# Kernel tuning notes

Measured on AMD Instinct MI355X. Metric: run time of the kernel, lower is better.

The kernel has to match this reference:

```python
import jax, jax.numpy as jnp
import numpy as np

N_HEAD = 12
SCALING = 0.17677669529663687  # 1/sqrt(head_dim=32)


def setup_inputs() -> dict:
    key = jax.random.key(0)
    ks = jax.random.split(key, 6)
    B, R, C, E = 1, 256, 384, 384
    s = 1.0 / np.sqrt(E)
    return {
        "x": jax.random.normal(ks[0], (B, R, C, E), dtype=jnp.float32),
        "Wq": (jax.random.normal(ks[1], (E, E), dtype=jnp.float32) * s),
        "Wk": (jax.random.normal(ks[2], (E, E), dtype=jnp.float32) * s),
        "Wv": (jax.random.normal(ks[3], (E, E), dtype=jnp.float32) * s),
        "Wq_s": (jax.random.normal(ks[4], (E, E), dtype=jnp.float32) * s),
        "Wk_s": (jax.random.normal(ks[5], (E, E), dtype=jnp.float32) * s),
        "res_mask": jnp.ones((B, C), dtype=jnp.int32),
        "seq_mask": jnp.ones((B, R), dtype=jnp.int32),
    }


def reference(x, Wq, Wk, Wv, Wq_s, Wk_s, res_mask, seq_mask):
    B, R, C, E = x.shape
    H = N_HEAD
    D = E // H
    NEG = jnp.finfo(x.dtype).min

    # ---- SeqWeightAttention: per-column attention over rows, query = row 0 ----
    scale_s = 1.0 / np.sqrt(D)
    msa = jnp.transpose(x, (0, 2, 1, 3))                 # [B,C,R,E]
    q0 = msa[:, :, 0]                                    # [B,C,E]
    Qs = (q0 @ Wq_s).reshape(B, C, 1, H, D)
    Qs = jnp.transpose(Qs, (0, 1, 3, 2, 4)) * scale_s    # [B,C,H,1,D]
    Ks = (msa @ Wk_s).reshape(B, C, R, H, D)
    Ks = jnp.transpose(Ks, (0, 1, 3, 4, 2))              # [B,C,H,D,R]
    QKs = Qs @ Ks                                        # [B,C,H,1,R]
    QKs = jnp.where(seq_mask[:, None, None, None, :] == 0, NEG, QKs)
    sw = jax.nn.softmax(QKs, axis=-1)
    sw = jnp.transpose(sw, (0, 4, 1, 2, 3))              # [B,R,C,H,1]

    # ---- main attention, row-contracted (attn_seq_weight path) ----
    scaling = SCALING / np.sqrt(C)                        # seqlen_scaling=True
    Q = (x @ Wq).reshape(B, R, C, H, D) * scaling * sw    # Q modulated by seq weights
    K = (x @ Wk).reshape(B, R, C, H, D)
    V = (x @ Wv).reshape(B, R, C, H, D)

    QK = jnp.einsum('brihd,brjhd->bhij', Q, K)            # contract rows + head_dim
    rm = res_mask[:, :, None] * res_mask[:, None, :]      # [B,C,C]
    QK = jnp.where(rm[:, None, :, :] == 0, NEG, QK)
    attn = jax.nn.softmax(QK, axis=-1)                    # [B,H,C,C]

    out = jnp.einsum('bhij,brjhd->brihd', attn, V)
    return out.reshape(B, R, C, E)
```

## Files before the change

kernel.cpp:

```cpp
#include <hip/hip_runtime.h>
#include <math.h>
#include <stdint.h>

#define DEV_INLINE __device__ __forceinline__

constexpr int R_ = 256, C_ = 384, E_ = 384, H_ = 12, D_ = 32;
constexpr float NEGF = -3.402823466e38f;

typedef __attribute__((ext_vector_type(4))) float f32x4;
typedef __attribute__((ext_vector_type(8))) short short8;
typedef __attribute__((ext_vector_type(4))) unsigned short u16x4;

constexpr size_t o_qs     = 0;
constexpr size_t o_p      = o_qs + (size_t)C_ * E_;
constexpr size_t o_logits = o_p + (size_t)C_ * H_ * E_;
constexpr size_t o_sw     = o_logits + (size_t)C_ * H_ * R_;
constexpr size_t o_attn   = o_sw + (size_t)C_ * H_ * R_;
constexpr size_t o_q3     = o_attn + (size_t)H_ * C_ * C_;
constexpr size_t SZBIG  = 75497472;
constexpr size_t ob_q3b = o_q3 * 4;
constexpr size_t ob_k3b = ob_q3b + SZBIG;
constexpr size_t ob_v3b = ob_k3b + SZBIG;
constexpr size_t ob_xb  = ob_v3b + SZBIG;
constexpr size_t QKSZ   = 7077888;

DEV_INLINE unsigned short bf16h(float x) {
  unsigned int u = __builtin_bit_cast(unsigned int, x);
  unsigned int r = (u + 0x7FFFu + ((u >> 16) & 1u)) >> 16;
  return (unsigned short)r;
}
DEV_INLINE float waveRedMax(float v) {
#pragma unroll
  for (int o = 32; o > 0; o >>= 1) v = fmaxf(v, __shfl_down(v, o));
  return v;
}
DEV_INLINE float waveRedSum(float v) {
#pragma unroll
  for (int o = 32; o > 0; o >>= 1) v += __shfl_down(v, o);
  return v;
}

DEV_INLINE void gll16(const void* g, void* l) {
  __builtin_amdgcn_global_load_lds(
      reinterpret_cast<__attribute__((address_space(1))) void*>(
          reinterpret_cast<uintptr_t>(g)),
      reinterpret_cast<__attribute__((address_space(3))) void*>(
          reinterpret_cast<uintptr_t>(l)),
      16, 0, 0);
}

template <int ROWS, int UPR, int MASK, int SHIFT>
DEV_INLINE void stageT(const unsigned short* __restrict__ g, int lda,
                       unsigned short* l) {
  int t = threadIdx.x, w = t >> 6, lane = t & 63;
  constexpr int NI = (ROWS * UPR) / 64;
  constexpr int PW = NI / 4;
#pragma unroll
  for (int j = 0; j < PW; ++j) {
    int u0 = (w * PW + j) * 64;
    int u = u0 + lane;
    int row = u / UPR, qp = u % UPR;
    int q = qp ^ ((row >> SHIFT) & MASK);
    gll16(g + (size_t)row * lda + q * 8, l + (size_t)u0 * 8);
  }
}

template <int MASK, int SHIFT>
DEV_INLINE short8 fragLd(const unsigned short* base, int row, int q, int rowShorts) {
  int qp = q ^ ((row >> SHIFT) & MASK);
  return *(const short8*)(base + row * rowShorts + qp * 8);
}

__global__ void k_prep(const float* __restrict__ x, const float* __restrict__ Wq,
                       const float* __restrict__ Wk, const float* __restrict__ Wv,
                       unsigned short* __restrict__ xb, unsigned short* __restrict__ Wtb) {
  int bid = blockIdx.x, t = threadIdx.x;
  if (bid < 6144) {
    size_t i = ((size_t)bid * 384 + t) * 16;
    unsigned short h[16];
#pragma unroll
    for (int j = 0; j < 4; ++j) {
      float4 f = *(const float4*)&x[i + j * 4];
      h[j * 4 + 0] = bf16h(f.x);
      h[j * 4 + 1] = bf16h(f.y);
      h[j * 4 + 2] = bf16h(f.z);
      h[j * 4 + 3] = bf16h(f.w);
    }
    *(short8*)&xb[i] = *(const short8*)&h[0];
    *(short8*)&xb[i + 8] = *(const short8*)&h[8];
  } else {
    int n = bid - 6144;
    const float* W;
    int col;
    if (n < 384)      { W = Wq; col = n; }
    else if (n < 768) { W = Wk; col = n - 384; }
    else              { W = Wv; col = n - 768; }
    Wtb[(size_t)n * 384 + t] = bf16h(W[(size_t)t * 384 + col]);
  }
}

__global__ __launch_bounds__(256) void k_logits_sm(
    const float* __restrict__ x, const unsigned short* __restrict__ xb,
    const float* __restrict__ Wq_s, const float* __restrict__ Wk_s,
    const int* __restrict__ seq_mask, float* __restrict__ swT) {
  int c = blockIdx.x, t = threadIdx.x;
  __shared__ float xq[384], qs_l[384];
  __shared__ unsigned short pB[16 * 392];
  __shared__ unsigned short sA[256 * 32];
  __shared__ float lg[12 * 256];
  __shared__ float red[4];
  int w = t >> 6, lane = t & 63, id16 = lane & 15, g = lane >> 4;

  for (int k = t; k < 384; k += 256) xq[k] = x[(size_t)c * 384 + k];
  __syncthreads();
  for (int e = t; e < 384; e += 256) {
    float s = 0.f;
    for (int k = 0; k < 384; ++k) s += xq[k] * Wq_s[(size_t)k * 384 + e];
    qs_l[e] = s * 0.17677669529663687f;
  }
  __syncthreads();
  for (int idx = t; idx < 4608; idx += 256) {
    int h = idx / 384, kk = idx - h * 384;
    const float* wrow = &Wk_s[(size_t)kk * 384 + h * 32];
    const float* qv = &qs_l[h * 32];
    float s = 0.f;
#pragma unroll
    for (int d = 0; d < 32; d += 4) {
      float4 wv = *(const float4*)&wrow[d];
      s += wv.x * qv[d] + wv.y * qv[d + 1] + wv.z * qv[d + 2] + wv.w * qv[d + 3];
    }
    pB[h * 392 + kk] = bf16h(s);
  }
  for (int i = t + 12 * 392; i < 16 * 392; i += 256) pB[i] = 0;
  __syncthreads();

  f32x4 acc[4];
#pragma unroll
  for (int mi = 0; mi < 4; ++mi) acc[mi] = (f32x4){0.f, 0.f, 0.f, 0.f};
  for (int k0 = 0; k0 < 384; k0 += 32) {
    stageT<256, 4, 3, 0>(xb + (size_t)c * 384 + k0, 384 * 384, sA);
    __syncthreads();
    short8 Bf = *(const short8*)(pB + id16 * 392 + k0 + g * 8);
#pragma unroll
    for (int mi = 0; mi < 4; ++mi) {
      short8 Af = fragLd<3, 0>(sA, w * 64 + mi * 16 + id16, g, 32);
      acc[mi] = __builtin_amdgcn_mfma_f32_16x16x32_bf16(Af, Bf, acc[mi], 0, 0, 0);
    }
    __syncthreads();
  }
  int l4 = (lane >> 4) * 4;
#pragma unroll
  for (int mi = 0; mi < 4; ++mi) {
    if (id16 < 12) {
      f32x4 a = acc[mi];
#pragma unroll
      for (int reg = 0; reg < 4; ++reg)
        lg[id16 * 256 + w * 64 + mi * 16 + l4 + reg] = a[reg];
    }
  }
  __syncthreads();
  int wid = t >> 6;
  const float scal = 0.17677669529663687f / sqrtf((float)C_);
  bool masked = (seq_mask[t] == 0);
  for (int h = 0; h < 12; ++h) {
    float v = masked ? NEGF : lg[h * 256 + t];
    float m = waveRedMax(v);
    if ((t & 63) == 0) red[wid] = m;
    __syncthreads();
    float mx = fmaxf(fmaxf(red[0], red[1]), fmaxf(red[2], red[3]));
    __syncthreads();
    float e = expf(v - mx);
    float s = waveRedSum(e);
    if ((t & 63) == 0) red[wid] = s;
    __syncthreads();
    float sum = red[0] + red[1] + red[2] + red[3];
    swT[((size_t)h * 256 + t) * 384 + c] = e / sum * scal;
    __syncthreads();
  }
}

__global__ __launch_bounds__(256, 4) void k_proj_all(
    const unsigned short* __restrict__ xb, const unsigned short* __restrict__ Wtb,
    const float* __restrict__ swT, unsigned short* __restrict__ Q3b,
    unsigned short* __restrict__ K3b, unsigned short* __restrict__ V3b) {
  __shared__ __align__(16) unsigned short smem[2 * 128 * 64];
  unsigned short* sA = smem;
  unsigned short* sB = smem + 128 * 64;
  int Dd = blockIdx.x;
  int L = (Dd & 7) * 864 + (Dd >> 3);
  int bm = L / 9, bn = L - bm * 9;
  int n0 = bn * 128, m0 = bm * 128;
  int wave = threadIdx.x >> 6, wr = wave >> 1, wc = wave & 1;
  int lane = threadIdx.x & 63, id16 = lane & 15, g = lane >> 4;
  f32x4 acc[4][4];
#pragma unroll
  for (int mi = 0; mi < 4; ++mi)
#pragma unroll
    for (int ni = 0; ni < 4; ++ni) acc[mi][ni] = (f32x4){0.f, 0.f, 0.f, 0.f};

  for (int it = 0; it < 6; ++it) {
    stageT<128, 8, 7, 0>(xb + (size_t)m0 * 384 + it * 64, 384, sA);
    stageT<128, 8, 7, 0>(Wtb + (size_t)n0 * 384 + it * 64, 384, sB);
    __syncthreads();
    short8 Af[4][2], Bf[4][2];
#pragma unroll
    for (int mi = 0; mi < 4; ++mi) {
      int row = wr * 64 + mi * 16 + id16;
#pragma unroll
      for (int kk = 0; kk < 2; ++kk) Af[mi][kk] = fragLd<7, 0>(sA, row, kk * 4 + g, 64);
    }
#pragma unroll
    for (int ni = 0; ni < 4; ++ni) {
      int col = wc * 64 + ni * 16 + id16;
#pragma unroll
      for (int kk = 0; kk < 2; ++kk) Bf[ni][kk] = fragLd<7, 0>(sB, col, kk * 4 + g, 64);
    }
#pragma unroll
    for (int kk = 0; kk < 2; ++kk)
#pragma unroll
      for (int mi = 0; mi < 4; ++mi)
#pragma unroll
        for (int ni = 0; ni < 4; ++ni)
          acc[mi][ni] = __builtin_amdgcn_mfma_f32_16x16x32_bf16(Af[mi][kk], Bf[ni][kk],
                                                                acc[mi][ni], 0, 0, 0);
    __syncthreads();
  }

  int l4 = (lane >> 4) * 4;
  int r = bm / 3, cb = (bm % 3) * 128;
  if (bn < 6) {
    bool isQ = bn < 3;
    int hbase = isQ ? bn * 4 : (bn - 3) * 4;
#pragma unroll
    for (int mi = 0; mi < 4; ++mi) {
      int clBase = wr * 64 + mi * 16 + l4;
#pragma unroll
      for (int ni = 0; ni < 4; ++ni) {
        int nl = wc * 64 + ni * 16 + id16;
        int hhl = nl >> 5, d = nl & 31;
        f32x4 a = acc[mi][ni];
        if (isQ) {
          float4 sv =
              *(const float4*)&swT[((size_t)(hbase + hhl) * 256 + r) * 384 + cb + clBase];
          a[0] *= sv.x; a[1] *= sv.y; a[2] *= sv.z; a[3] *= sv.w;
        }
#pragma unroll
        for (int reg = 0; reg < 4; ++reg)
          smem[hhl * 4096 + (clBase + reg) * 32 + d] = bf16h(a[reg]);
      }
    }
    __syncthreads();
    unsigned short* dst = isQ ? Q3b : K3b;
#pragma unroll
    for (int seg = 0; seg < 8; ++seg) {
      int off = seg * 2048 + threadIdx.x * 8;
      int hhl = off >> 12, inner = off & 4095;
      int hg = hbase + hhl;
      *(short8*)(dst + (((size_t)hg * 256 + r) * 384 + cb) * 32 + inner) =
          *(const short8*)(smem + off);
    }
  } else {
    int hbase = (bn - 6) * 4;
#pragma unroll
    for (int mi = 0; mi < 4; ++mi) {
      int clBase = wr * 64 + mi * 16 + l4;
#pragma unroll
      for (int ni = 0; ni < 4; ++ni) {
        int nl = wc * 64 + ni * 16 + id16;
        int hhl = nl >> 5, d = nl & 31;
        int cg = clBase ^ ((d & 7) << 2);
        f32x4 a = acc[mi][ni];
        u16x4 hv;
#pragma unroll
        for (int reg = 0; reg < 4; ++reg) hv[reg] = bf16h(a[reg]);
        *(u16x4*)(smem + hhl * 4096 + d * 128 + cg) = hv;
      }
    }
    __syncthreads();
#pragma unroll
    for (int seg = 0; seg < 16; ++seg) {
      int Lg = seg * 1024 + threadIdx.x * 4;
      int hhl = Lg >> 12, rem = Lg & 4095, d = rem >> 7, cc = rem & 127;
      int cp = cc ^ ((d & 7) << 2);
      u16x4 v = *(const u16x4*)(smem + hhl * 4096 + d * 128 + cp);
      int hg = hbase + hhl;
      *(u16x4*)(V3b + ((size_t)hg * 8192 + r * 32 + d) * 384 + cb + cc) = v;
    }
  }
}

__global__ __launch_bounds__(256, 4) void k_qk_mma(
    const unsigned short* __restrict__ Q3b, const unsigned short* __restrict__ K3b,
    float* __restrict__ QKf0, float* __restrict__ QKf1,
    float* __restrict__ QKf2, float* __restrict__ QKf3) {
  __shared__ unsigned short sA[2 * 4096], sB[2 * 4096];
  int Dd = blockIdx.x;
  int L = (Dd & 7) * 54 + (Dd >> 3);
  int kh = L / 108, rem = L - kh * 108;
  int h = rem / 9, r2 = rem - h * 9, bi = r2 / 3, bj = r2 - bi * 3;
  int i0 = bi * 128, j0 = bj * 128;
  int wave = threadIdx.x >> 6, wr = wave >> 1, wc = wave & 1;
  int lane = threadIdx.x & 63, id16 = lane & 15, g = lane >> 4;
  f32x4 acc[4][4];
#pragma unroll
  for (int mi = 0; mi < 4; ++mi)
#pragma unroll
    for (int ni = 0; ni < 4; ++ni) acc[mi][ni] = (f32x4){0.f, 0.f, 0.f, 0.f};

  for (int it = 0; it < 32; ++it) {
    int r = kh * 64 + it * 2;
#pragma unroll
    for (int rr = 0; rr < 2; ++rr) {
      stageT<128, 4, 3, 1>(Q3b + (((size_t)h * 256 + r + rr) * 384 + i0) * 32, 32,
                           sA + rr * 4096);
      stageT<128, 4, 3, 1>(K3b + (((size_t)h * 256 + r + rr) * 384 + j0) * 32, 32,
                           sB + rr * 4096);
    }
    __syncthreads();
#pragma unroll
    for (int rr = 0; rr < 2; ++rr) {
      short8 Af[4], Bf[4];
#pragma unroll
      for (int mi = 0; mi < 4; ++mi)
        Af[mi] = fragLd<3, 1>(sA + rr * 4096, wr * 64 + mi * 16 + id16, g, 32);
#pragma unroll
      for (int ni = 0; ni < 4; ++ni)
        Bf[ni] = fragLd<3, 1>(sB + rr * 4096, wc * 64 + ni * 16 + id16, g, 32);
#pragma unroll
      for (int mi = 0; mi < 4; ++mi)
#pragma unroll
        for (int ni = 0; ni < 4; ++ni)
          acc[mi][ni] = __builtin_amdgcn_mfma_f32_16x16x32_bf16(Af[mi], Bf[ni],
                                                                acc[mi][ni], 0, 0, 0);
    }
    __syncthreads();
  }
  int l4 = (lane >> 4) * 4;
  float* dst = (kh == 0) ? QKf0 : (kh == 1) ? QKf1 : (kh == 2) ? QKf2 : QKf3;
#pragma unroll
  for (int mi = 0; mi < 4; ++mi)
#pragma unroll
    for (int ni = 0; ni < 4; ++ni) {
      int ii = i0 + wr * 64 + mi * 16 + l4;
      int j = j0 + wc * 64 + ni * 16 + id16;
      f32x4 a = acc[mi][ni];
#pragma unroll
      for (int reg = 0; reg < 4; ++reg)
        dst[((size_t)h * 384 + ii + reg) * 384 + j] = a[reg];
    }
}

__global__ void k_softmax_j(const int* __restrict__ res_mask, const float* __restrict__ QKf0,
                            const float* __restrict__ QKf1, const float* __restrict__ QKf2,
                            const float* __restrict__ QKf3,
                            unsigned short* __restrict__ attnb) {
  int i = blockIdx.x, h = blockIdx.y, t = threadIdx.x;
  int lane = t & 63, wid = t >> 6;
  size_t base = ((size_t)h * C_ + i) * C_;
  float v = (QKf0[base + t] + QKf1[base + t]) + (QKf2[base + t] + QKf3[base + t]);
  if ((res_mask[i] * res_mask[t]) == 0) v = NEGF;
  __shared__ float red[6];
  float m = waveRedMax(v);
  if (lane == 0) red[wid] = m;
  __syncthreads();
  float mx = red[0];
#pragma unroll
  for (int w = 1; w < 6; ++w) mx = fmaxf(mx, red[w]);
  __syncthreads();
  float e = expf(v - mx);
  float s = waveRedSum(e);
  if (lane == 0) red[wid] = s;
  __syncthreads();
  float sum = 0.f;
#pragma unroll
  for (int w = 0; w < 6; ++w) sum += red[w];
  attnb[base + t] = bf16h(e / sum);
}

__global__ __launch_bounds__(256, 4) void k_out_mma(
    const unsigned short* __restrict__ attnb, const unsigned short* __restrict__ V3b,
    float* __restrict__ out) {
  __shared__ __align__(16) unsigned short smem[2 * 128 * 64];
  unsigned short* sA = smem;
  unsigned short* sB = smem + 128 * 64;
  int Dd = blockIdx.x;
  int L = (Dd & 7) * 288 + (Dd >> 3);
  int bn = L % 64, bm = (L / 64) % 3, h = L / 192;
  int n0 = bn * 128, m0 = bm * 128;
  int wave = threadIdx.x >> 6, wr = wave >> 1, wc = wave & 1;
  int lane = threadIdx.x & 63, id16 = lane & 15, g = lane >> 4;
  f32x4 acc[4][4];
#pragma unroll
  for (int mi = 0; mi < 4; ++mi)
#pragma unroll
    for (int ni = 0; ni < 4; ++ni) acc[mi][ni] = (f32x4){0.f, 0.f, 0.f, 0.f};
  const unsigned short* Ab = attnb + (size_t)h * 384 * 384 + (size_t)m0 * 384;
  const unsigned short* Bb = V3b + (size_t)h * 8192 * 384 + (size_t)n0 * 384;

  for (int it = 0; it < 6; ++it) {
    stageT<128, 8, 7, 0>(Ab + it * 64, 384, sA);
    stageT<128, 8, 7, 0>(Bb + it * 64, 384, sB);
    __syncthreads();
    short8 Af[4][2], Bf[4][2];
#pragma unroll
    for (int mi = 0; mi < 4; ++mi) {
      int row = wr * 64 + mi * 16 + id16;
#pragma unroll
      for (int kk = 0; kk < 2; ++kk) Af[mi][kk] = fragLd<7, 0>(sA, row, kk * 4 + g, 64);
    }
#pragma unroll
    for (int ni = 0; ni < 4; ++ni) {
      int col = wc * 64 + ni * 16 + id16;
#pragma unroll
      for (int kk = 0; kk < 2; ++kk) Bf[ni][kk] = fragLd<7, 0>(sB, col, kk * 4 + g, 64);
    }
#pragma unroll
    for (int kk = 0; kk < 2; ++kk)
#pragma unroll
      for (int mi = 0; mi < 4; ++mi)
#pragma unroll
        for (int ni = 0; ni < 4; ++ni)
          acc[mi][ni] = __builtin_amdgcn_mfma_f32_16x16x32_bf16(Af[mi][kk], Bf[ni][kk],
                                                                acc[mi][ni], 0, 0, 0);
    __syncthreads();
  }

  int l4 = (lane >> 4) * 4;
  float* smf = (float*)smem;
#pragma unroll
  for (int p = 0; p < 2; ++p) {
#pragma unroll
    for (int mi = 0; mi < 4; ++mi) {
      int iL = wr * 64 + mi * 16 + l4;
#pragma unroll
      for (int nq = 0; nq < 2; ++nq) {
        int ni = 2 * p + nq;
        int d = nq * 16 + id16;
        f32x4 a = acc[mi][ni];
#pragma unroll
        for (int reg = 0; reg < 4; ++reg)
          smf[wc * 4096 + (iL + reg) * 32 + d] = a[reg];
      }
    }
    __syncthreads();
#pragma unroll
    for (int seg = 0; seg < 8; ++seg) {
      int o = seg * 1024 + threadIdx.x * 4;
      int plane = o >> 12, rest = o & 4095;
      int iL = rest >> 5, d = rest & 31;
      int rg = (n0 >> 5) + plane * 2 + p;
      *(float4*)&out[(((size_t)rg * 384 + m0 + iL) * 12 + h) * 32 + d] =
          *(const float4*)&smf[o];
    }
    __syncthreads();
  }
}

extern "C" void kernel_launch(void* const* d_in, const int* in_sizes, int n_in,
                              void* d_out, int out_size, void* d_ws, size_t ws_size,
                              hipStream_t stream) {
  const float* x = (const float*)d_in[0];
  const float* Wq = (const float*)d_in[1];
  const float* Wk = (const float*)d_in[2];
  const float* Wv = (const float*)d_in[3];
  const float* Wq_s = (const float*)d_in[4];
  const float* Wk_s = (const float*)d_in[5];
  const int* res_mask = (const int*)d_in[6];
  const int* seq_mask = (const int*)d_in[7];
  float* ws = (float*)d_ws;
  char* wsb = (char*)d_ws;
  float* out = (float*)d_out;

  float* swT          = ws + o_logits;
  unsigned short* Wtb = (unsigned short*)(wsb + o_attn * 4);
  float* QKf0         = ws + o_attn;
  unsigned short* Q3b = (unsigned short*)(wsb + ob_q3b);
  unsigned short* K3b = (unsigned short*)(wsb + ob_k3b);
  unsigned short* V3b = (unsigned short*)(wsb + ob_v3b);
  unsigned short* xb  = (unsigned short*)(wsb + ob_xb);
  unsigned short* attnb = Q3b;
  float* QKf1 = (float*)(wsb + ob_xb);
  float* QKf2 = (float*)(wsb + ob_xb + QKSZ);
  float* QKf3 = (float*)(wsb + ob_xb + 2 * QKSZ);

  hipLaunchKernelGGL(k_prep, dim3(7296), dim3(384), 0, stream, x, Wq, Wk, Wv, xb, Wtb);
  hipLaunchKernelGGL(k_logits_sm, dim3(C_), dim3(256), 0, stream, x, xb, Wq_s, Wk_s,
                     seq_mask, swT);
  hipLaunchKernelGGL(k_proj_all, dim3(6912), dim3(256), 0, stream, xb, Wtb, swT,
                     Q3b, K3b, V3b);
  hipLaunchKernelGGL(k_qk_mma, dim3(432), dim3(256), 0, stream, Q3b, K3b,
                     QKf0, QKf1, QKf2, QKf3);
  hipLaunchKernelGGL(k_softmax_j, dim3(C_, H_), dim3(C_), 0, stream, res_mask,
                     QKf0, QKf1, QKf2, QKf3, attnb);
  hipLaunchKernelGGL(k_out_mma, dim3(2304), dim3(256), 0, stream, attnb, V3b, out);
}
```

Measured before the change: 358.5 us.

## Store QK partials as bf16 and retile out GEMM to full-row attention tiles

The QK split-K partial sums are now written as bf16 rather than fp32, which halves the traffic between the QK kernel and the softmax kernel. The cost is extra rounding error on the logits before they are summed. The output GEMM is also retiled: each block now keeps all 384 attention rows in LDS against a 64-column slice of V, with 32-wide K steps and a 6x4 accumulator per wave. This stops re-reading V tiles across row blocks, but it uses more registers and lowers launch bounds occupancy to 3.

```diff
diff --git a/kernel.cpp b/kernel.cpp
--- a/kernel.cpp
+++ b/kernel.cpp
@@ -11,9 +11,7 @@
 typedef __attribute__((ext_vector_type(8))) short short8;
 typedef __attribute__((ext_vector_type(4))) unsigned short u16x4;
 
-constexpr size_t o_qs     = 0;
-constexpr size_t o_p      = o_qs + (size_t)C_ * E_;
-constexpr size_t o_logits = o_p + (size_t)C_ * H_ * E_;
+constexpr size_t o_logits = (size_t)C_ * E_ + (size_t)C_ * H_ * E_;
 constexpr size_t o_sw     = o_logits + (size_t)C_ * H_ * R_;
 constexpr size_t o_attn   = o_sw + (size_t)C_ * H_ * R_;
 constexpr size_t o_q3     = o_attn + (size_t)H_ * C_ * C_;
@@ -22,12 +20,15 @@
 constexpr size_t ob_k3b = ob_q3b + SZBIG;
 constexpr size_t ob_v3b = ob_k3b + SZBIG;
 constexpr size_t ob_xb  = ob_v3b + SZBIG;
-constexpr size_t QKSZ   = 7077888;
+constexpr size_t PSZ    = 3538944;
 
 DEV_INLINE unsigned short bf16h(float x) {
   unsigned int u = __builtin_bit_cast(unsigned int, x);
   unsigned int r = (u + 0x7FFFu + ((u >> 16) & 1u)) >> 16;
   return (unsigned short)r;
+}
+DEV_INLINE float b2f(unsigned short u) {
+  return __builtin_bit_cast(float, ((unsigned int)u) << 16);
 }
 DEV_INLINE float waveRedMax(float v) {
 #pragma unroll
@@ -291,8 +292,8 @@
 
 __global__ __launch_bounds__(256, 4) void k_qk_mma(
     const unsigned short* __restrict__ Q3b, const unsigned short* __restrict__ K3b,
-    float* __restrict__ QKf0, float* __restrict__ QKf1,
-    float* __restrict__ QKf2, float* __restrict__ QKf3) {
+    unsigned short* __restrict__ P0, unsigned short* __restrict__ P1,
+    unsigned short* __restrict__ P2, unsigned short* __restrict__ P3) {
   __shared__ unsigned short sA[2 * 4096], sB[2 * 4096];
   int Dd = blockIdx.x;
   int L = (Dd & 7) * 54 + (Dd >> 3);
@@ -336,7 +337,7 @@
     __syncthreads();
   }
   int l4 = (lane >> 4) * 4;
-  float* dst = (kh == 0) ? QKf0 : (kh == 1) ? QKf1 : (kh == 2) ? QKf2 : QKf3;
+  unsigned short* dst = (kh == 0) ? P0 : (kh == 1) ? P1 : (kh == 2) ? P2 : P3;
 #pragma unroll
   for (int mi = 0; mi < 4; ++mi)
 #pragma unroll
@@ -346,18 +347,21 @@
       f32x4 a = acc[mi][ni];
 #pragma unroll
       for (int reg = 0; reg < 4; ++reg)
-        dst[((size_t)h * 384 + ii + reg) * 384 + j] = a[reg];
-    }
-}
-
-__global__ void k_softmax_j(const int* __restrict__ res_mask, const float* __restrict__ QKf0,
-                            const float* __restrict__ QKf1, const float* __restrict__ QKf2,
-                            const float* __restrict__ QKf3,
+        dst[((size_t)h * 384 + ii + reg) * 384 + j] = bf16h(a[reg]);
+    }
+}
+
+__global__ void k_softmax_j(const int* __restrict__ res_mask,
+                            const unsigned short* __restrict__ P0,
+                            const unsigned short* __restrict__ P1,
+                            const unsigned short* __restrict__ P2,
+                            const unsigned short* __restrict__ P3,
                             unsigned short* __restrict__ attnb) {
   int i = blockIdx.x, h = blockIdx.y, t = threadIdx.x;
   int lane = t & 63, wid = t >> 6;
   size_t base = ((size_t)h * C_ + i) * C_;
-  float v = (QKf0[base + t] + QKf1[base + t]) + (QKf2[base + t] + QKf3[base + t]);
+  float v = (b2f(P0[base + t]) + b2f(P1[base + t])) +
+            (b2f(P2[base + t]) + b2f(P3[base + t]));
   if ((res_mask[i] * res_mask[t]) == 0) v = NEGF;
   __shared__ float red[6];
   float m = waveRedMax(v);
@@ -377,79 +381,71 @@
   attnb[base + t] = bf16h(e / sum);
 }
 
-__global__ __launch_bounds__(256, 4) void k_out_mma(
+__global__ __launch_bounds__(256, 3) void k_out_mma(
     const unsigned short* __restrict__ attnb, const unsigned short* __restrict__ V3b,
     float* __restrict__ out) {
-  __shared__ __align__(16) unsigned short smem[2 * 128 * 64];
+  __shared__ __align__(16) unsigned short smem[16384];
   unsigned short* sA = smem;
-  unsigned short* sB = smem + 128 * 64;
+  unsigned short* sB = smem + 12288;
   int Dd = blockIdx.x;
-  int L = (Dd & 7) * 288 + (Dd >> 3);
-  int bn = L % 64, bm = (L / 64) % 3, h = L / 192;
-  int n0 = bn * 128, m0 = bm * 128;
-  int wave = threadIdx.x >> 6, wr = wave >> 1, wc = wave & 1;
+  int L = (Dd & 7) * 192 + (Dd >> 3);
+  int h = L >> 7, rdt = L & 127;
+  int w = threadIdx.x >> 6;
   int lane = threadIdx.x & 63, id16 = lane & 15, g = lane >> 4;
-  f32x4 acc[4][4];
-#pragma unroll
-  for (int mi = 0; mi < 4; ++mi)
-#pragma unroll
-    for (int ni = 0; ni < 4; ++ni) acc[mi][ni] = (f32x4){0.f, 0.f, 0.f, 0.f};
-  const unsigned short* Ab = attnb + (size_t)h * 384 * 384 + (size_t)m0 * 384;
-  const unsigned short* Bb = V3b + (size_t)h * 8192 * 384 + (size_t)n0 * 384;
-
-  for (int it = 0; it < 6; ++it) {
-    stageT<128, 8, 7, 0>(Ab + it * 64, 384, sA);
-    stageT<128, 8, 7, 0>(Bb + it * 64, 384, sB);
-    __syncthreads();
-    short8 Af[4][2], Bf[4][2];
-#pragma unroll
-    for (int mi = 0; mi < 4; ++mi) {
-      int row = wr * 64 + mi * 16 + id16;
-#pragma unroll
-      for (int kk = 0; kk < 2; ++kk) Af[mi][kk] = fragLd<7, 0>(sA, row, kk * 4 + g, 64);
-    }
-#pragma unroll
-    for (int ni = 0; ni < 4; ++ni) {
-      int col = wc * 64 + ni * 16 + id16;
-#pragma unroll
-      for (int kk = 0; kk < 2; ++kk) Bf[ni][kk] = fragLd<7, 0>(sB, col, kk * 4 + g, 64);
-    }
-#pragma unroll
-    for (int kk = 0; kk < 2; ++kk)
-#pragma unroll
-      for (int mi = 0; mi < 4; ++mi)
-#pragma unroll
-        for (int ni = 0; ni < 4; ++ni)
-          acc[mi][ni] = __builtin_amdgcn_mfma_f32_16x16x32_bf16(Af[mi][kk], Bf[ni][kk],
-                                                                acc[mi][ni], 0, 0, 0);
+  f32x4 acc[6][4];
+#pragma unroll
+  for (int mi = 0; mi < 6; ++mi)
+#pragma unroll
+    for (int nf = 0; nf < 4; ++nf) acc[mi][nf] = (f32x4){0.f, 0.f, 0.f, 0.f};
+  const unsigned short* Ab = attnb + (size_t)h * 147456;
+  const unsigned short* Bb = V3b + (size_t)h * 8192 * 384 + (size_t)(rdt * 64) * 384;
+
+  for (int it = 0; it < 12; ++it) {
+    stageT<384, 4, 3, 1>(Ab + it * 32, 384, sA);
+    stageT<64, 4, 3, 1>(Bb + it * 32, 384, sB);
+    __syncthreads();
+    short8 Af[6], Bf[4];
+#pragma unroll
+    for (int mi = 0; mi < 6; ++mi)
+      Af[mi] = fragLd<3, 1>(sA, w * 96 + mi * 16 + id16, g, 32);
+#pragma unroll
+    for (int nf = 0; nf < 4; ++nf)
+      Bf[nf] = fragLd<3, 1>(sB, nf * 16 + id16, g, 32);
+#pragma unroll
+    for (int mi = 0; mi < 6; ++mi)
+#pragma unroll
+      for (int nf = 0; nf < 4; ++nf)
+        acc[mi][nf] = __builtin_amdgcn_mfma_f32_16x16x32_bf16(Af[mi], Bf[nf],
+                                                              acc[mi][nf], 0, 0, 0);
     __syncthreads();
   }
 
   int l4 = (lane >> 4) * 4;
   float* smf = (float*)smem;
 #pragma unroll
-  for (int p = 0; p < 2; ++p) {
-#pragma unroll
-    for (int mi = 0; mi < 4; ++mi) {
-      int iL = wr * 64 + mi * 16 + l4;
-#pragma unroll
-      for (int nq = 0; nq < 2; ++nq) {
-        int ni = 2 * p + nq;
-        int d = nq * 16 + id16;
-        f32x4 a = acc[mi][ni];
+  for (int p = 0; p < 3; ++p) {
+#pragma unroll
+    for (int mi = 0; mi < 6; ++mi) {
+      int rb = w * 96 + mi * 16;
+      if ((rb >> 7) != p) continue;
+      int ibase = (rb & 127) + l4;
+#pragma unroll
+      for (int nf = 0; nf < 4; ++nf) {
+        int rdl = nf * 16 + id16;
+        f32x4 a = acc[mi][nf];
 #pragma unroll
         for (int reg = 0; reg < 4; ++reg)
-          smf[wc * 4096 + (iL + reg) * 32 + d] = a[reg];
+          smf[(ibase + reg) * 64 + rdl] = a[reg];
       }
     }
     __syncthreads();
 #pragma unroll
     for (int seg = 0; seg < 8; ++seg) {
       int o = seg * 1024 + threadIdx.x * 4;
-      int plane = o >> 12, rest = o & 4095;
-      int iL = rest >> 5, d = rest & 31;
-      int rg = (n0 >> 5) + plane * 2 + p;
-      *(float4*)&out[(((size_t)rg * 384 + m0 + iL) * 12 + h) * 32 + d] =
+      int il = o >> 6, rdl = o & 63;
+      int rg = rdt * 2 + (rdl >> 5), d = rdl & 31;
+      int i = p * 128 + il;
+      *(float4*)&out[(((size_t)rg * 384 + i) * 12 + h) * 32 + d] =
           *(const float4*)&smf[o];
     }
     __syncthreads();
@@ -473,24 +469,23 @@
 
   float* swT          = ws + o_logits;
   unsigned short* Wtb = (unsigned short*)(wsb + o_attn * 4);
-  float* QKf0         = ws + o_attn;
   unsigned short* Q3b = (unsigned short*)(wsb + ob_q3b);
   unsigned short* K3b = (unsigned short*)(wsb + ob_k3b);
   unsigned short* V3b = (unsigned short*)(wsb + ob_v3b);
   unsigned short* xb  = (unsigned short*)(wsb + ob_xb);
   unsigned short* attnb = Q3b;
-  float* QKf1 = (float*)(wsb + ob_xb);
-  float* QKf2 = (float*)(wsb + ob_xb + QKSZ);
-  float* QKf3 = (float*)(wsb + ob_xb + 2 * QKSZ);
+  unsigned short* P0 = (unsigned short*)(wsb + ob_xb);
+  unsigned short* P1 = (unsigned short*)(wsb + ob_xb + PSZ);
+  unsigned short* P2 = (unsigned short*)(wsb + ob_xb + 2 * PSZ);
+  unsigned short* P3 = (unsigned short*)(wsb + ob_xb + 3 * PSZ);
 
   hipLaunchKernelGGL(k_prep, dim3(7296), dim3(384), 0, stream, x, Wq, Wk, Wv, xb, Wtb);
   hipLaunchKernelGGL(k_logits_sm, dim3(C_), dim3(256), 0, stream, x, xb, Wq_s, Wk_s,
                      seq_mask, swT);
   hipLaunchKernelGGL(k_proj_all, dim3(6912), dim3(256), 0, stream, xb, Wtb, swT,
                      Q3b, K3b, V3b);
-  hipLaunchKernelGGL(k_qk_mma, dim3(432), dim3(256), 0, stream, Q3b, K3b,
-                     QKf0, QKf1, QKf2, QKf3);
+  hipLaunchKernelGGL(k_qk_mma, dim3(432), dim3(256), 0, stream, Q3b, K3b, P0, P1, P2, P3);
   hipLaunchKernelGGL(k_softmax_j, dim3(C_, H_), dim3(C_), 0, stream, res_mask,
-                     QKf0, QKf1, QKf2, QKf3, attnb);
-  hipLaunchKernelGGL(k_out_mma, dim3(2304), dim3(256), 0, stream, attnb, V3b, out);
-}
+                     P0, P1, P2, P3, attnb);
+  hipLaunchKernelGGL(k_out_mma, dim3(1536), dim3(256), 0, stream, attnb, V3b, out);
+}
```

Result: no change. 357.2 us (-0.4%).
